# Performance work log

Hardware: AMD Instinct MI355X
Metric: run time of the kernel (lower is better)

Reference implementation:

```python
import jax, jax.numpy as jnp
import numpy as np

W, H = 256, 256          # image width (x) and height (y); image indexed [x, y] like the torch code
N = 8192                 # depth-sorted visible gaussians
TILE = 16                # tile_size default
CHUNK = 128              # gaussians composited per scan step (N % CHUNK == 0)
MIN_WEIGHT = 1e-6        # early-termination threshold from render_pixel


def setup_inputs() -> dict:
    key = jax.random.key(0)
    k1, k2, k3, k4, k5 = jax.random.split(key, 5)
    # pixel-space means, uniformly over the image
    points_xy = jax.random.uniform(k1, (N, 2), dtype=jnp.float32) * jnp.array([W, H], jnp.float32)
    # SPD inverse 2D covariances: Sigma = R diag(var) R^T, inv = R diag(1/var) R^T
    theta = jax.random.uniform(k2, (N,), dtype=jnp.float32) * (2.0 * np.pi)
    sig = jax.random.uniform(k3, (N, 2), dtype=jnp.float32, minval=1.5, maxval=8.0)
    var = sig ** 2
    ct, st = jnp.cos(theta), jnp.sin(theta)
    R = jnp.stack([jnp.stack([ct, -st], -1), jnp.stack([st, ct], -1)], -2)  # [N,2,2]
    inverse_covariance = jnp.einsum('nij,nj,nkj->nik', R, 1.0 / var, R)
    # radius = ceil(2.5 * sqrt(max eigenvalue)) as in compute_radius
    radius = jnp.ceil(2.5 * jnp.sqrt(jnp.max(var, axis=1)))
    colors = jax.random.uniform(k4, (N, 3), dtype=jnp.float32)
    opacity = jax.random.normal(k5, (N,), dtype=jnp.float32)  # pre-sigmoid logits
    return dict(points_xy=points_xy, inverse_covariance=inverse_covariance,
                radius=radius, colors=colors, opacity=opacity)


def _rasterize(points_xy, inverse_covariance, radius, colors, opacity):
    px = jnp.arange(W, dtype=jnp.float32)[:, None]   # [W,1] pixel x coords
    py = jnp.arange(H, dtype=jnp.float32)[None, :]   # [1,H] pixel y coords
    # tile origin for each pixel (tile-based culling as in render_image)
    tile_x0 = ((jnp.arange(W) // TILE) * TILE).astype(jnp.float32)[:, None]  # [W,1]
    tile_y0 = ((jnp.arange(H) // TILE) * TILE).astype(jnp.float32)[None, :]  # [1,H]
    # per-gaussian bounding boxes (preprocess)
    min_x = jnp.floor(points_xy[:, 0] - radius); max_x = jnp.ceil(points_xy[:, 0] + radius)
    min_y = jnp.floor(points_xy[:, 1] - radius); max_y = jnp.ceil(points_xy[:, 1] + radius)

    n_chunks = N // CHUNK
    def chunk(a):
        return a.reshape((n_chunks, CHUNK) + a.shape[1:])
    xs = dict(mx=chunk(points_xy[:, 0]), my=chunk(points_xy[:, 1]),
              a=chunk(inverse_covariance[:, 0, 0]), b=chunk(inverse_covariance[:, 0, 1]),
              c=chunk(inverse_covariance[:, 1, 1]),
              mnx=chunk(min_x), mxx=chunk(max_x), mny=chunk(min_y), mxy=chunk(max_y),
              col=chunk(colors), op=chunk(opacity))

    @jax.checkpoint
    def body(carry, ch):
        T, color = carry  # T: [W,H] remaining transmittance; color: [W,H,3]
        dx = px[None] - ch['mx'][:, None, None]  # [C,W,1]
        dy = py[None] - ch['my'][:, None, None]  # [C,1,H]
        # mahalanobis form d^T Sigma^{-1} d with symmetric inv cov [[a,b],[b,c]]
        q = (ch['a'][:, None, None] * dx * dx
             + 2.0 * ch['b'][:, None, None] * dx * dy
             + ch['c'][:, None, None] * dy * dy)              # [C,W,H]
        alpha = jnp.exp(-0.5 * q) * jax.nn.sigmoid(ch['op'])[:, None, None]
        # gaussian participates for a pixel iff its bbox intersects that pixel's tile
        in_tile = ((ch['mnx'][:, None, None] <= tile_x0[None] + TILE)
                   & (ch['mxx'][:, None, None] >= tile_x0[None])
                   & (ch['mny'][:, None, None] <= tile_y0[None] + TILE)
                   & (ch['mxy'][:, None, None] >= tile_y0[None]))   # [C,W,H]
        alpha = jnp.where(in_tile, alpha, 0.0)
        cum = jnp.cumprod(1.0 - alpha, axis=0)                 # inclusive prefix of (1-alpha)
        T_before = T[None] * jnp.concatenate([jnp.ones_like(cum[:1]), cum[:-1]], axis=0)
        # original: test_weight = T_before*(1-alpha); terminate (skip contribution) if < min_weight
        include = (T[None] * cum) >= MIN_WEIGHT
        contrib = jnp.where(include, T_before * alpha, 0.0)   # [C,W,H]
        color = color + jnp.einsum('cwh,cd->whd', contrib, ch['col'])
        return (T * cum[-1], color), None

    init = (jnp.ones((W, H), jnp.float32), jnp.zeros((W, H, 3), jnp.float32))
    (_, color), _ = jax.lax.scan(body, init, xs)
    return color  # [W,H,3] image indexed [x,y]


def reference(points_xy, inverse_covariance, radius, colors, opacity):
    return _rasterize(points_xy, inverse_covariance, radius, colors, opacity)
```

## Files before the change

kernel.cpp:

```cpp
#include <hip/hip_runtime.h>
#include <hip/hip_fp16.h>

#define WIDTH   256
#define HEIGHT  256
#define NG      8192
#define TILE_SZ 16
#define MINW    1e-6f
#define BLK     1024
#define NBATCH  (NG / BLK)
#define NWAVE   (BLK / 64)
#define NSEG    16
#define PXB     128
#define RSZ     512
#define KC      (-0.72134752044f)

__global__ __launch_bounds__(BLK, 8) void raster_kernel(
    const float* __restrict__ pts,
    const float* __restrict__ icov,
    const float* __restrict__ rad,
    const float* __restrict__ cols,
    const float* __restrict__ opac,
    float* __restrict__ out)
{
    __shared__ unsigned long long s_ball[NBATCH * NWAVE];
    __shared__ int s_pfx[NBATCH * NWAVE];
    __shared__ __align__(16) char s_pool[32768];
    unsigned short* s_list = (unsigned short*)s_pool;
    float4* s_g = (float4*)(s_pool + 16384);
    float*  s_red = (float*)s_pool;
    __shared__ float s_P[NSEG][PXB];

    const int tid  = threadIdx.x;
    const int lane = tid & 63;
    const int wave = tid >> 6;
    const int seg  = wave;
    const float tx0 = (float)(blockIdx.x * TILE_SZ);
    const float ty0 = (float)(blockIdx.y * TILE_SZ);
    const float tx1 = tx0 + (float)TILE_SZ;
    const float ty1 = ty0 + (float)TILE_SZ;

    unsigned int hitbits = 0;
    #pragma unroll
    for (int b = 0; b < NBATCH; ++b) {
        const int g = b * BLK + tid;
        const float2 p = ((const float2*)pts)[g];
        const float  r = rad[g];
        bool hit = (floorf(p.x - r) <= tx1) & (ceilf(p.x + r) >= tx0)
                 & (floorf(p.y - r) <= ty1) & (ceilf(p.y + r) >= ty0);
        unsigned long long m = __ballot(hit);
        if (lane == 0) s_ball[b * NWAVE + wave] = m;
        if (hit) hitbits |= (1u << b);
    }
    __syncthreads();
    if (wave == 0) {
        int v0 = __popcll(s_ball[lane]);
        int v1 = __popcll(s_ball[64 + lane]);
        #pragma unroll
        for (int d = 1; d < 64; d <<= 1) {
            const int t0 = __shfl_up(v0, d);
            const int t1 = __shfl_up(v1, d);
            if (lane >= d) { v0 += t0; v1 += t1; }
        }
        s_pfx[lane] = v0;
        s_pfx[64 + lane] = v1 + __shfl(v0, 63);
    }
    __syncthreads();
    const int count = s_pfx[127];
    {
        unsigned int hb = hitbits;
        const unsigned long long ltmask = (1ull << lane) - 1ull;
        while (hb) {
            const int b = __ffs(hb) - 1;  hb &= hb - 1;
            const int idx = b * NWAVE + wave;
            const unsigned long long m = s_ball[idx];
            const int bs = idx ? s_pfx[idx - 1] : 0;
            s_list[bs + __popcll(m & ltmask)] = (unsigned short)(b * BLK + tid);
        }
    }
    __syncthreads();

    const int pr = tid & 63;
    const int xl = pr >> 3, yp = pr & 7;
    const float fx  = tx0 + (float)(blockIdx.z * 8 + xl);
    const float fyA = ty0 + (float)(2 * yp);
    const int pA = xl * 16 + 2 * yp;
    const int pxi[2] = {pA, pA + 1};
    float Tpx = 1.0f;
    float acc[3][2];
    #pragma unroll
    for (int c = 0; c < 3; ++c) { acc[c][0] = 0.0f; acc[c][1] = 0.0f; }

    for (int base = 0; base < count; base += RSZ) {
        const int n = min(RSZ, count - base);
        if (tid < n) {
            const int g = s_list[base + tid];
            const float2 p = ((const float2*)pts)[g];
            const float4 ic = ((const float4*)icov)[g];
            const float op = 1.0f / (1.0f + __expf(-opac[g]));
            const __half2 h = __floats2half2_rn(cols[3 * g], cols[3 * g + 1]);
            unsigned rgbits; __builtin_memcpy(&rgbits, &h, 4);
            s_g[tid * 2 + 0] = make_float4(p.x, p.y, KC * ic.x, 2.0f * KC * ic.y);
            s_g[tid * 2 + 1] = make_float4(KC * ic.w, op, __uint_as_float(rgbits),
                                           cols[3 * g + 2]);
        }
        __syncthreads();

        const int L  = (n + NSEG - 1) >> 4;
        const int i0 = seg * L;
        const int i1 = min(i0 + L, n);

        float P[2] = {1.f, 1.f};
        float l[3][2];
        #pragma unroll
        for (int c = 0; c < 3; ++c) { l[c][0] = 0.0f; l[c][1] = 0.0f; }

        #pragma unroll 2
        for (int i = i0; i < i1; ++i) {
            const float4 g0 = s_g[i * 2 + 0];
            const float4 g1 = s_g[i * 2 + 1];
            const float dx  = fx - g0.x;
            const float axx = (g0.z * dx) * dx;
            const float bdx = g0.w * dx;
            const float dyA = fyA - g0.y, dyB = dyA + 1.0f;
            const float qv[2] = { fmaf(dyA, fmaf(g1.x, dyA, bdx), axx),
                                  fmaf(dyB, fmaf(g1.x, dyB, bdx), axx) };
            const unsigned rgbits = __float_as_uint(g1.z);
            __half2 h; __builtin_memcpy(&h, &rgbits, 4);
            const float2 rg = __half22float2(h);
            #pragma unroll
            for (int k = 0; k < 2; ++k) {
                const float a = g1.y * __builtin_amdgcn_exp2f(qv[k]);
                const float w = P[k] * a;
                l[0][k] = fmaf(w, rg.x, l[0][k]);
                l[1][k] = fmaf(w, rg.y, l[1][k]);
                l[2][k] = fmaf(w, g1.w, l[2][k]);
                P[k] = fmaf(-a, P[k], P[k]);
            }
        }
        s_P[seg][pxi[0]] = P[0];
        s_P[seg][pxi[1]] = P[1];
        __syncthreads();

        if (tid < PXB) {
            float run = Tpx;
            #pragma unroll
            for (int s = 0; s < NSEG; ++s) {
                const float Pv = s_P[s][tid];
                s_P[s][tid] = run;
                run *= Pv;
            }
            Tpx = run;
        }
        __syncthreads();

        float Tin[2];
        bool gated[2]; bool anyg = false;
        #pragma unroll
        for (int k = 0; k < 2; ++k) {
            Tin[k] = s_P[seg][pxi[k]];
            const bool alive = (Tin[k] >= MINW);
            gated[k] = alive && (Tin[k] * P[k] < MINW);
            if (alive && !gated[k]) {
                acc[0][k] = fmaf(Tin[k], l[0][k], acc[0][k]);
                acc[1][k] = fmaf(Tin[k], l[1][k], acc[1][k]);
                acc[2][k] = fmaf(Tin[k], l[2][k], acc[2][k]);
            }
            anyg |= gated[k];
        }
        if (__ballot(anyg) != 0ull) {
            float Tl[2] = {Tin[0], Tin[1]};
            for (int i = i0; i < i1; ++i) {
                const float4 g0 = s_g[i * 2 + 0];
                const float4 g1 = s_g[i * 2 + 1];
                const float dx  = fx - g0.x;
                const float axx = (g0.z * dx) * dx;
                const float bdx = g0.w * dx;
                const float dyA = fyA - g0.y, dyB = dyA + 1.0f;
                const float qv[2] = { fmaf(dyA, fmaf(g1.x, dyA, bdx), axx),
                                      fmaf(dyB, fmaf(g1.x, dyB, bdx), axx) };
                const unsigned rgbits = __float_as_uint(g1.z);
                __half2 h; __builtin_memcpy(&h, &rgbits, 4);
                const float2 rg = __half22float2(h);
                #pragma unroll
                for (int k = 0; k < 2; ++k) {
                    const float a  = g1.y * __builtin_amdgcn_exp2f(qv[k]);
                    const float Tn = Tl[k] * (1.0f - a);
                    const float w  = (gated[k] && Tn >= MINW) ? Tl[k] * a : 0.0f;
                    acc[0][k] = fmaf(w, rg.x, acc[0][k]);
                    acc[1][k] = fmaf(w, rg.y, acc[1][k]);
                    acc[2][k] = fmaf(w, g1.w, acc[2][k]);
                    Tl[k] = Tn;
                }
            }
        }
        const bool mydead = (tid < PXB) ? (Tpx < MINW) : true;
        if (__syncthreads_count(mydead) == BLK) break;
    }

    #pragma unroll
    for (int k = 0; k < 2; ++k) {
        s_red[(seg * PXB + pxi[k]) * 3 + 0] = acc[0][k];
        s_red[(seg * PXB + pxi[k]) * 3 + 1] = acc[1][k];
        s_red[(seg * PXB + pxi[k]) * 3 + 2] = acc[2][k];
    }
    __syncthreads();
    if (tid < PXB * 3) {
        const int p  = tid / 3;
        const int ch = tid - 3 * p;
        float v = 0.0f;
        #pragma unroll
        for (int s = 0; s < NSEG; ++s) v += s_red[(s * PXB + p) * 3 + ch];
        const int x = blockIdx.x * TILE_SZ + blockIdx.z * 8 + (p >> 4);
        const int y = blockIdx.y * TILE_SZ + (p & 15);
        out[(x * HEIGHT + y) * 3 + ch] = v;
    }
}

extern "C" void kernel_launch(void* const* d_in, const int* in_sizes, int n_in,
                              void* d_out, int out_size, void* d_ws, size_t ws_size,
                              hipStream_t stream) {
    const float* pts  = (const float*)d_in[0];
    const float* icov = (const float*)d_in[1];
    const float* rad  = (const float*)d_in[2];
    const float* cols = (const float*)d_in[3];
    const float* opac = (const float*)d_in[4];
    float* out = (float*)d_out;
    dim3 grid(WIDTH / TILE_SZ, HEIGHT / TILE_SZ, 2);
    raster_kernel<<<grid, dim3(BLK), 0, stream>>>(pts, icov, rad, cols, opac, out);
}
```

Baseline: 78.10 us.

## Precompute per-gaussian table and bounding boxes in a separate prep kernel

Adds a prep kernel that computes, once per gaussian, the packed shading record (scaled inverse covariance, sigmoid opacity, half-packed color) and the float4 bounding box, writing both into workspace. The raster kernel then reads bounding boxes directly for culling and copies table entries into shared memory, instead of redoing the sigmoid, pack and floor/ceil work in each of the 512 blocks. It also skips the barrier-count termination check on the last batch and changes the final reduction to a two-phase 8-segment shared-memory sum. The cost is an extra kernel launch and a workspace round-trip.

After: 80.16 us. 2.6% more time.

```diff
diff --git a/kernel.cpp b/kernel.cpp
--- a/kernel.cpp
+++ b/kernel.cpp
@@ -14,12 +14,29 @@
 #define RSZ     512
 #define KC      (-0.72134752044f)
 
+__global__ __launch_bounds__(256) void prep_kernel(
+    const float* __restrict__ pts, const float* __restrict__ icov,
+    const float* __restrict__ cols, const float* __restrict__ opac,
+    const float* __restrict__ rad,
+    float4* __restrict__ table, float4* __restrict__ bbt)
+{
+    const int g = blockIdx.x * 256 + threadIdx.x;
+    const float2 p = ((const float2*)pts)[g];
+    const float4 ic = ((const float4*)icov)[g];
+    const float r  = rad[g];
+    const float op = 1.0f / (1.0f + __expf(-opac[g]));
+    const __half2 h = __floats2half2_rn(cols[3 * g], cols[3 * g + 1]);
+    unsigned rgbits; __builtin_memcpy(&rgbits, &h, 4);
+    table[2 * g + 0] = make_float4(p.x, p.y, KC * ic.x, 2.0f * KC * ic.y);
+    table[2 * g + 1] = make_float4(KC * ic.w, op, __uint_as_float(rgbits),
+                                   cols[3 * g + 2]);
+    bbt[g] = make_float4(floorf(p.x - r), ceilf(p.x + r),
+                         floorf(p.y - r), ceilf(p.y + r));
+}
+
 __global__ __launch_bounds__(BLK, 8) void raster_kernel(
-    const float* __restrict__ pts,
-    const float* __restrict__ icov,
-    const float* __restrict__ rad,
-    const float* __restrict__ cols,
-    const float* __restrict__ opac,
+    const float4* __restrict__ bbt,
+    const float4* __restrict__ table,
     float* __restrict__ out)
 {
     __shared__ unsigned long long s_ball[NBATCH * NWAVE];
@@ -27,7 +44,7 @@
     __shared__ __align__(16) char s_pool[32768];
     unsigned short* s_list = (unsigned short*)s_pool;
     float4* s_g = (float4*)(s_pool + 16384);
-    float*  s_red = (float*)s_pool;
+    float*  pool = (float*)s_pool;
     __shared__ float s_P[NSEG][PXB];
 
     const int tid  = threadIdx.x;
@@ -42,11 +59,8 @@
     unsigned int hitbits = 0;
     #pragma unroll
     for (int b = 0; b < NBATCH; ++b) {
-        const int g = b * BLK + tid;
-        const float2 p = ((const float2*)pts)[g];
-        const float  r = rad[g];
-        bool hit = (floorf(p.x - r) <= tx1) & (ceilf(p.x + r) >= tx0)
-                 & (floorf(p.y - r) <= ty1) & (ceilf(p.y + r) >= ty0);
+        const float4 bb = bbt[b * BLK + tid];
+        bool hit = (bb.x <= tx1) & (bb.y >= tx0) & (bb.z <= ty1) & (bb.w >= ty0);
         unsigned long long m = __ballot(hit);
         if (lane == 0) s_ball[b * NWAVE + wave] = m;
         if (hit) hitbits |= (1u << b);
@@ -84,7 +98,7 @@
     const float fx  = tx0 + (float)(blockIdx.z * 8 + xl);
     const float fyA = ty0 + (float)(2 * yp);
     const int pA = xl * 16 + 2 * yp;
-    const int pxi[2] = {pA, pA + 1};
+    const int pB = pA + 1;
     float Tpx = 1.0f;
     float acc[3][2];
     #pragma unroll
@@ -94,14 +108,8 @@
         const int n = min(RSZ, count - base);
         if (tid < n) {
             const int g = s_list[base + tid];
-            const float2 p = ((const float2*)pts)[g];
-            const float4 ic = ((const float4*)icov)[g];
-            const float op = 1.0f / (1.0f + __expf(-opac[g]));
-            const __half2 h = __floats2half2_rn(cols[3 * g], cols[3 * g + 1]);
-            unsigned rgbits; __builtin_memcpy(&rgbits, &h, 4);
-            s_g[tid * 2 + 0] = make_float4(p.x, p.y, KC * ic.x, 2.0f * KC * ic.y);
-            s_g[tid * 2 + 1] = make_float4(KC * ic.w, op, __uint_as_float(rgbits),
-                                           cols[3 * g + 2]);
+            s_g[tid * 2 + 0] = table[2 * g + 0];
+            s_g[tid * 2 + 1] = table[2 * g + 1];
         }
         __syncthreads();
 
@@ -137,8 +145,8 @@
                 P[k] = fmaf(-a, P[k], P[k]);
             }
         }
-        s_P[seg][pxi[0]] = P[0];
-        s_P[seg][pxi[1]] = P[1];
+        s_P[seg][pA] = P[0];
+        s_P[seg][pB] = P[1];
         __syncthreads();
 
         if (tid < PXB) {
@@ -157,7 +165,7 @@
         bool gated[2]; bool anyg = false;
         #pragma unroll
         for (int k = 0; k < 2; ++k) {
-            Tin[k] = s_P[seg][pxi[k]];
+            Tin[k] = s_P[seg][k ? pB : pA];
             const bool alive = (Tin[k] >= MINW);
             gated[k] = alive && (Tin[k] * P[k] < MINW);
             if (alive && !gated[k]) {
@@ -193,15 +201,30 @@
                 }
             }
         }
-        const bool mydead = (tid < PXB) ? (Tpx < MINW) : true;
-        if (__syncthreads_count(mydead) == BLK) break;
-    }
-
-    #pragma unroll
-    for (int k = 0; k < 2; ++k) {
-        s_red[(seg * PXB + pxi[k]) * 3 + 0] = acc[0][k];
-        s_red[(seg * PXB + pxi[k]) * 3 + 1] = acc[1][k];
-        s_red[(seg * PXB + pxi[k]) * 3 + 2] = acc[2][k];
+        if (base + RSZ < count) {
+            const bool mydead = (tid < PXB) ? (Tpx < MINW) : true;
+            if (__syncthreads_count(mydead) == BLK) break;
+        }
+    }
+    __syncthreads();
+
+    const int s8 = seg & 7;
+    if (seg < 8) {
+        pool[(s8 * PXB + pA) * 3 + 0] = acc[0][0];
+        pool[(s8 * PXB + pA) * 3 + 1] = acc[1][0];
+        pool[(s8 * PXB + pA) * 3 + 2] = acc[2][0];
+        pool[(s8 * PXB + pB) * 3 + 0] = acc[0][1];
+        pool[(s8 * PXB + pB) * 3 + 1] = acc[1][1];
+        pool[(s8 * PXB + pB) * 3 + 2] = acc[2][1];
+    }
+    __syncthreads();
+    if (seg >= 8) {
+        pool[(s8 * PXB + pA) * 3 + 0] += acc[0][0];
+        pool[(s8 * PXB + pA) * 3 + 1] += acc[1][0];
+        pool[(s8 * PXB + pA) * 3 + 2] += acc[2][0];
+        pool[(s8 * PXB + pB) * 3 + 0] += acc[0][1];
+        pool[(s8 * PXB + pB) * 3 + 1] += acc[1][1];
+        pool[(s8 * PXB + pB) * 3 + 2] += acc[2][1];
     }
     __syncthreads();
     if (tid < PXB * 3) {
@@ -209,7 +232,7 @@
         const int ch = tid - 3 * p;
         float v = 0.0f;
         #pragma unroll
-        for (int s = 0; s < NSEG; ++s) v += s_red[(s * PXB + p) * 3 + ch];
+        for (int s = 0; s < 8; ++s) v += pool[(s * PXB + p) * 3 + ch];
         const int x = blockIdx.x * TILE_SZ + blockIdx.z * 8 + (p >> 4);
         const int y = blockIdx.y * TILE_SZ + (p & 15);
         out[(x * HEIGHT + y) * 3 + ch] = v;
@@ -225,6 +248,9 @@
     const float* cols = (const float*)d_in[3];
     const float* opac = (const float*)d_in[4];
     float* out = (float*)d_out;
+    float4* table = (float4*)d_ws;
+    float4* bbt   = table + 2 * NG;
+    prep_kernel<<<NG / 256, 256, 0, stream>>>(pts, icov, cols, opac, rad, table, bbt);
     dim3 grid(WIDTH / TILE_SZ, HEIGHT / TILE_SZ, 2);
-    raster_kernel<<<grid, dim3(BLK), 0, stream>>>(pts, icov, rad, cols, opac, out);
+    raster_kernel<<<grid, dim3(BLK), 0, stream>>>(bbt, table, out);
 }
```
